# Kernel optimization log

Measured on AMD Instinct MI355X. Metric: run time of the kernel, lower is better.

The kernel has to match this reference:

```python
import jax, jax.numpy as jnp
import numpy as np

B, N = 64, 512
D_ENT, H = 2000, 768
LN_EPS = 1e-12


def setup_inputs() -> dict:
    key = jax.random.key(0)
    ks = jax.random.split(key, 16)
    s = 1.0 / np.sqrt(D_ENT)
    sh = 1.0 / np.sqrt(H)
    return {
        "node_embeddings": jax.random.normal(ks[0], (B, N, D_ENT), jnp.float32),
        "node_types": jax.random.randint(ks[1], (B, N), 0, 2),
        "layers": jax.random.randint(ks[2], (B, N), 0, 8),
        "operators": jax.random.randint(ks[3], (B, N), 0, 2),
        "in_degs": jax.random.randint(ks[4], (B, N), 0, 8),
        "out_degs": jax.random.randint(ks[5], (B, N), 0, 8),
        "negs": jax.random.randint(ks[6], (B, N), 0, 2),
        "type_emb": jax.random.normal(ks[7], (2, H), jnp.float32),
        "layer_emb": jax.random.normal(ks[8], (8, H), jnp.float32),
        "op_emb": jax.random.normal(ks[9], (2, H), jnp.float32),
        "in_emb": jax.random.normal(ks[10], (8, H), jnp.float32),
        "out_emb": jax.random.normal(ks[11], (8, H), jnp.float32),
        "proj_w": jax.random.uniform(ks[12], (H, D_ENT), jnp.float32, -s, s),
        "proj_b": jnp.zeros((H,), jnp.float32),
        "neg_w": jax.random.uniform(ks[13], (H, H), jnp.float32, -sh, sh),
        "neg_b": jnp.zeros((H,), jnp.float32),
        "ln_g": jnp.ones((H,), jnp.float32),
        "ln_b": jnp.zeros((H,), jnp.float32),
    }


def reference(node_embeddings, node_types, layers, operators, in_degs, out_degs, negs,
              type_emb, layer_emb, op_emb, in_emb, out_emb,
              proj_w, proj_b, neg_w, neg_b, ln_g, ln_b):
    # linear projection: [B,N,D_ENT] @ [D_ENT,H]
    x = jnp.einsum("bnd,hd->bnh", node_embeddings, proj_w) + proj_b
    # summed small-table lookups
    x = x + type_emb[node_types] + layer_emb[layers] + op_emb[operators] \
        + in_emb[in_degs] + out_emb[out_degs]
    # rows with negs==1 go through MLP (single Linear h->h); masked select/scatter
    y = jnp.einsum("bnh,gh->bng", x, neg_w) + neg_b
    x = jnp.where((negs == 1)[..., None], y, x)
    # LayerNorm
    mu = jnp.mean(x, axis=-1, keepdims=True)
    var = jnp.mean(jnp.square(x - mu), axis=-1, keepdims=True)
    x = (x - mu) * jax.lax.rsqrt(var + LN_EPS) * ln_g + ln_b
    # dropout is identity in eval mode
    return x
```

## Files before the change

kernel.cpp:

```cpp
#include <hip/hip_runtime.h>
#include <stdint.h>

typedef unsigned short u16;
typedef short v8s __attribute__((ext_vector_type(8)));
typedef float v4f __attribute__((ext_vector_type(4)));

typedef __attribute__((address_space(1))) uint32_t g_u32;
typedef __attribute__((address_space(3))) uint32_t l_u32;

__device__ __forceinline__ void glds16(const void* g, void* l) {
    __builtin_amdgcn_global_load_lds((const g_u32*)g, (l_u32*)l, 16, 0, 0);
}

__device__ __forceinline__ u16 f2b(float f) {
    uint32_t u = __builtin_bit_cast(uint32_t, f);
    u += 0x7FFFu + ((u >> 16) & 1u);
    return (u16)(u >> 16);
}

__device__ __forceinline__ uint32_t pk2(float a, float b) {
    uint32_t ua = __builtin_bit_cast(uint32_t, a) + 0x8000u;
    uint32_t ub = __builtin_bit_cast(uint32_t, b) + 0x8000u;
    return __builtin_amdgcn_perm(ub, ua, 0x07060302u);
}

#define MTOT  32768
#define HDIM  768
#define KDIM  2000
#define KPAD  2016

__global__ __launch_bounds__(256) void cvt_weights(
    const float* __restrict__ pw, const float* __restrict__ nw,
    u16* __restrict__ Wb, u16* __restrict__ NWb)
{
    const int h = blockIdx.x;
    const float* src = pw + (size_t)h * KDIM;
    u16* dst = Wb + (size_t)h * KPAD;
    for (int k = threadIdx.x; k < KPAD; k += 256)
        dst[k] = (k < KDIM) ? f2b(src[k]) : (u16)0;
    const float* s2 = nw + (size_t)h * HDIM;
    u16* d2 = NWb + (size_t)h * HDIM;
    for (int k = threadIdx.x; k < HDIM; k += 256)
        d2[k] = f2b(s2[k]);
}

__global__ __launch_bounds__(256, 3) void gemm1(
    const float* __restrict__ A, const u16* __restrict__ Wb,
    const float* __restrict__ pb,
    const int* __restrict__ i_ty, const int* __restrict__ i_la,
    const int* __restrict__ i_op, const int* __restrict__ i_in, const int* __restrict__ i_ou,
    const float* __restrict__ te, const float* __restrict__ le, const float* __restrict__ oe,
    const float* __restrict__ ie, const float* __restrict__ ooe,
    u16* __restrict__ Xb)
{
    __shared__ __align__(16) float Asf[128 * 32];
    __shared__ __align__(16) u16  Bs[128 * 32];

    const int bid = blockIdx.x;
    const int slot = bid >> 3;
    const int mt = (bid & 7) * 32 + slot / 6;
    const int nt = slot % 6;
    const int m_base = mt * 128, n_base = nt * 128;

    const int tid = threadIdx.x;
    const int w = tid >> 6, lane = tid & 63;
    const int lm = lane & 15, quad = lane >> 4;
    const int wm = (w >> 1) * 64, wn = (w & 1) * 64;

    const float* aRowBase[4];
    int aChunkOff[4];
    float* aDst[4];
#pragma unroll
    for (int t = 0; t < 4; t++) {
        const int rl = w * 32 + t * 8 + (lane >> 3);
        const int c16 = (lane & 7) ^ (rl & 7);
        aRowBase[t] = A + (size_t)(m_base + rl) * KDIM;
        aChunkOff[t] = c16 * 4;
        aDst[t] = &Asf[(w * 32 + t * 8) * 32];
    }
    const u16* bSrc[2];
    u16* bDst[2];
#pragma unroll
    for (int t = 0; t < 2; t++) {
        const int rl = w * 32 + t * 16 + (lane >> 2);
        const int c = (lane & 3) ^ ((rl >> 1) & 3);
        bSrc[t] = Wb + (size_t)(n_base + rl) * KPAD + c * 8;
        bDst[t] = &Bs[(w * 32 + t * 16) * 32];
    }

    v4f acc[4][4];
#pragma unroll
    for (int i = 0; i < 4; i++)
#pragma unroll
        for (int j = 0; j < 4; j++) acc[i][j] = (v4f){0.f, 0.f, 0.f, 0.f};

    for (int kb = 0; kb < KPAD / 32; ++kb) {
        __syncthreads();
#pragma unroll
        for (int t = 0; t < 4; t++) {
            int k = kb * 32 + aChunkOff[t];
            k = (k > 1996) ? 1996 : k;
            glds16(aRowBase[t] + k, aDst[t]);
        }
#pragma unroll
        for (int t = 0; t < 2; t++)
            glds16(bSrc[t] + kb * 32, bDst[t]);
        __syncthreads();

        v8s af[4], bf[4];
#pragma unroll
        for (int i = 0; i < 4; i++) {
            const int r = wm + i * 16 + lm;
            const int sw = r & 7;
            const float4 lo = *(const float4*)&Asf[r * 32 + (((2 * quad)     ^ sw) << 2)];
            const float4 hi = *(const float4*)&Asf[r * 32 + (((2 * quad + 1) ^ sw) << 2)];
            int4 p;
            p.x = (int)pk2(lo.x, lo.y); p.y = (int)pk2(lo.z, lo.w);
            p.z = (int)pk2(hi.x, hi.y); p.w = (int)pk2(hi.z, hi.w);
            af[i] = __builtin_bit_cast(v8s, p);
        }
#pragma unroll
        for (int j = 0; j < 4; j++) {
            const int r = wn + j * 16 + lm;
            bf[j] = *(const v8s*)&Bs[r * 32 + (quad ^ ((r >> 1) & 3)) * 8];
        }
#pragma unroll
        for (int i = 0; i < 4; i++)
#pragma unroll
            for (int j = 0; j < 4; j++)
                acc[i][j] = __builtin_amdgcn_mfma_f32_16x16x32_bf16(af[i], bf[j], acc[i][j], 0, 0, 0);
    }

#pragma unroll
    for (int i = 0; i < 4; i++) {
#pragma unroll
        for (int r = 0; r < 4; r++) {
            const int row = m_base + wm + i * 16 + quad * 4 + r;
            const int ty = i_ty[row], la = i_la[row], op = i_op[row];
            const int di = i_in[row], doo = i_ou[row];
            const float* pte = te + (size_t)ty * HDIM;
            const float* ple = le + (size_t)la * HDIM;
            const float* poe = oe + (size_t)op * HDIM;
            const float* pie = ie + (size_t)di * HDIM;
            const float* pou = ooe + (size_t)doo * HDIM;
            u16* orow = Xb + (size_t)row * HDIM;
#pragma unroll
            for (int j = 0; j < 4; j++) {
                const int col = n_base + wn + j * 16 + lm;
                float v = acc[i][j][r] + pb[col] + pte[col] + ple[col] + poe[col] + pie[col] + pou[col];
                orow[col] = f2b(v);
            }
        }
    }
}

__global__ __launch_bounds__(256, 3) void gemm2(
    const u16* __restrict__ Xb, const u16* __restrict__ NWb,
    const float* __restrict__ nb, u16* __restrict__ Yb)
{
    __shared__ __align__(16) u16 As[128 * 32];
    __shared__ __align__(16) u16 Bs[128 * 32];

    const int bid = blockIdx.x;
    const int slot = bid >> 3;
    const int mt = (bid & 7) * 32 + slot / 6;
    const int nt = slot % 6;
    const int m_base = mt * 128, n_base = nt * 128;

    const int tid = threadIdx.x;
    const int w = tid >> 6, lane = tid & 63;
    const int lm = lane & 15, quad = lane >> 4;
    const int wm = (w >> 1) * 64, wn = (w & 1) * 64;

    const u16* aSrc[2]; u16* aDst[2];
    const u16* bSrc[2]; u16* bDst[2];
#pragma unroll
    for (int t = 0; t < 2; t++) {
        const int rl = w * 32 + t * 16 + (lane >> 2);
        const int c = (lane & 3) ^ ((rl >> 1) & 3);
        aSrc[t] = Xb  + (size_t)(m_base + rl) * HDIM + c * 8;
        aDst[t] = &As[(w * 32 + t * 16) * 32];
        bSrc[t] = NWb + (size_t)(n_base + rl) * HDIM + c * 8;
        bDst[t] = &Bs[(w * 32 + t * 16) * 32];
    }

    v4f acc[4][4];
#pragma unroll
    for (int i = 0; i < 4; i++)
#pragma unroll
        for (int j = 0; j < 4; j++) acc[i][j] = (v4f){0.f, 0.f, 0.f, 0.f};

    for (int kb = 0; kb < HDIM / 32; ++kb) {
        __syncthreads();
#pragma unroll
        for (int t = 0; t < 2; t++) {
            glds16(aSrc[t] + kb * 32, aDst[t]);
            glds16(bSrc[t] + kb * 32, bDst[t]);
        }
        __syncthreads();

        v8s af[4], bf[4];
#pragma unroll
        for (int i = 0; i < 4; i++) {
            const int r = wm + i * 16 + lm;
            af[i] = *(const v8s*)&As[r * 32 + (quad ^ ((r >> 1) & 3)) * 8];
        }
#pragma unroll
        for (int j = 0; j < 4; j++) {
            const int r = wn + j * 16 + lm;
            bf[j] = *(const v8s*)&Bs[r * 32 + (quad ^ ((r >> 1) & 3)) * 8];
        }
#pragma unroll
        for (int i = 0; i < 4; i++)
#pragma unroll
            for (int j = 0; j < 4; j++)
                acc[i][j] = __builtin_amdgcn_mfma_f32_16x16x32_bf16(af[i], bf[j], acc[i][j], 0, 0, 0);
    }

#pragma unroll
    for (int i = 0; i < 4; i++) {
#pragma unroll
        for (int r = 0; r < 4; r++) {
            const int row = m_base + wm + i * 16 + quad * 4 + r;
            u16* orow = Yb + (size_t)row * HDIM;
#pragma unroll
            for (int j = 0; j < 4; j++) {
                const int col = n_base + wn + j * 16 + lm;
                orow[col] = f2b(acc[i][j][r] + nb[col]);
            }
        }
    }
}

__global__ __launch_bounds__(256) void ln_k(
    const u16* __restrict__ Xb, const u16* __restrict__ Yb,
    const int* __restrict__ negs,
    const float* __restrict__ g, const float* __restrict__ b,
    float* __restrict__ out)
{
    const int w = threadIdx.x >> 6, lane = threadIdx.x & 63;
    const int row = blockIdx.x * 4 + w;
    const u16* src = ((negs[row] == 1) ? Yb : Xb) + (size_t)row * HDIM;

    float v[12];
    float s = 0.f, ss = 0.f;
#pragma unroll
    for (int p = 0; p < 3; p++) {
        uint2 u = *(const uint2*)(src + (p * 64 + lane) * 4);
        float f0 = __builtin_bit_cast(float, u.x << 16);
        float f1 = __builtin_bit_cast(float, u.x & 0xFFFF0000u);
        float f2 = __builtin_bit_cast(float, u.y << 16);
        float f3 = __builtin_bit_cast(float, u.y & 0xFFFF0000u);
        v[p * 4 + 0] = f0; v[p * 4 + 1] = f1; v[p * 4 + 2] = f2; v[p * 4 + 3] = f3;
        s += f0 + f1 + f2 + f3;
        ss += f0 * f0 + f1 * f1 + f2 * f2 + f3 * f3;
    }
#pragma unroll
    for (int off = 1; off < 64; off <<= 1) {
        s += __shfl_xor(s, off);
        ss += __shfl_xor(ss, off);
    }
    const float mean = s * (1.f / (float)HDIM);
    const float var = ss * (1.f / (float)HDIM) - mean * mean;
    const float rs = rsqrtf(var + 1e-12f);

    float* orow = out + (size_t)row * HDIM;
#pragma unroll
    for (int p = 0; p < 3; p++) {
        const int c0 = (p * 64 + lane) * 4;
        float4 gg = *(const float4*)(g + c0);
        float4 bb = *(const float4*)(b + c0);
        float4 o;
        o.x = (v[p * 4 + 0] - mean) * rs * gg.x + bb.x;
        o.y = (v[p * 4 + 1] - mean) * rs * gg.y + bb.y;
        o.z = (v[p * 4 + 2] - mean) * rs * gg.z + bb.z;
        o.w = (v[p * 4 + 3] - mean) * rs * gg.w + bb.w;
        *(float4*)(orow + c0) = o;
    }
}

extern "C" void kernel_launch(void* const* d_in, const int* in_sizes, int n_in,
                              void* d_out, int out_size, void* d_ws, size_t ws_size,
                              hipStream_t stream) {
    (void)in_sizes; (void)n_in; (void)out_size; (void)ws_size;
    const float* A   = (const float*)d_in[0];
    const int* i_ty  = (const int*)d_in[1];
    const int* i_la  = (const int*)d_in[2];
    const int* i_op  = (const int*)d_in[3];
    const int* i_in  = (const int*)d_in[4];
    const int* i_ou  = (const int*)d_in[5];
    const int* negs  = (const int*)d_in[6];
    const float* te  = (const float*)d_in[7];
    const float* le  = (const float*)d_in[8];
    const float* oe  = (const float*)d_in[9];
    const float* ie  = (const float*)d_in[10];
    const float* ooe = (const float*)d_in[11];
    const float* pw  = (const float*)d_in[12];
    const float* pb  = (const float*)d_in[13];
    const float* nw  = (const float*)d_in[14];
    const float* nb  = (const float*)d_in[15];
    const float* lng = (const float*)d_in[16];
    const float* lnb = (const float*)d_in[17];
    float* out = (float*)d_out;

    char* ws = (char*)d_ws;
    u16* Wb  = (u16*)ws;
    u16* NWb = (u16*)(ws + 3096576);
    u16* Xb  = (u16*)(ws + 3096576 + 1179648);
    u16* Yb  = (u16*)(ws + 3096576 + 1179648 + 50331648);

    cvt_weights<<<768, 256, 0, stream>>>(pw, nw, Wb, NWb);
    gemm1<<<1536, 256, 0, stream>>>(A, Wb, pb, i_ty, i_la, i_op, i_in, i_ou,
                                    te, le, oe, ie, ooe, Xb);
    gemm2<<<1536, 256, 0, stream>>>(Xb, NWb, nb, Yb);
    ln_k<<<8192, 256, 0, stream>>>(Xb, Yb, negs, lng, lnb, out);
}
```

Baseline: 676.8 us.

## Pre-convert activations to bf16 in a separate pass before the projection GEMM

Adds a kernel that converts the fp32 node embeddings to bf16 in workspace. The projection GEMM then streams bf16 tiles straight into LDS and drops the per-iteration fp32-to-bf16 packing, halving both the A-tile LDS footprint and the global read volume across the N-tiles. The change also raises the occupancy hint from 3 to 4 for both GEMMs. The cost is an extra full read and write pass over the large input. The old fused path stays as a fallback when the workspace is too small.

```diff
diff --git a/kernel.cpp b/kernel.cpp
--- a/kernel.cpp
+++ b/kernel.cpp
@@ -28,6 +28,24 @@
 #define HDIM  768
 #define KDIM  2000
 #define KPAD  2016
+
+__global__ __launch_bounds__(256) void cvt_a(
+    const float* __restrict__ A, u16* __restrict__ Ab)
+{
+    const int t = threadIdx.x;
+    if (t >= 250) return;
+#pragma unroll
+    for (int r = 0; r < 8; r++) {
+        const int row = blockIdx.x * 8 + r;
+        const float* src = A + (size_t)row * KDIM + t * 8;
+        const float4 a = ((const float4*)src)[0];
+        const float4 b = ((const float4*)src)[1];
+        int4 p;
+        p.x = (int)pk2(a.x, a.y); p.y = (int)pk2(a.z, a.w);
+        p.z = (int)pk2(b.x, b.y); p.w = (int)pk2(b.z, b.w);
+        *(int4*)(Ab + (size_t)row * KDIM + t * 8) = p;
+    }
+}
 
 __global__ __launch_bounds__(256) void cvt_weights(
     const float* __restrict__ pw, const float* __restrict__ nw,
@@ -44,8 +62,8 @@
         d2[k] = f2b(s2[k]);
 }
 
-__global__ __launch_bounds__(256, 3) void gemm1(
-    const float* __restrict__ A, const u16* __restrict__ Wb,
+__global__ __launch_bounds__(256, 4) void gemm1(
+    const u16* __restrict__ Ab, const u16* __restrict__ Wb,
     const float* __restrict__ pb,
     const int* __restrict__ i_ty, const int* __restrict__ i_la,
     const int* __restrict__ i_op, const int* __restrict__ i_in, const int* __restrict__ i_ou,
@@ -53,8 +71,8 @@
     const float* __restrict__ ie, const float* __restrict__ ooe,
     u16* __restrict__ Xb)
 {
-    __shared__ __align__(16) float Asf[128 * 32];
-    __shared__ __align__(16) u16  Bs[128 * 32];
+    __shared__ __align__(16) u16 As[128 * 32];
+    __shared__ __align__(16) u16 Bs[128 * 32];
 
     const int bid = blockIdx.x;
     const int slot = bid >> 3;
@@ -67,25 +85,17 @@
     const int lm = lane & 15, quad = lane >> 4;
     const int wm = (w >> 1) * 64, wn = (w & 1) * 64;
 
-    const float* aRowBase[4];
-    int aChunkOff[4];
-    float* aDst[4];
-#pragma unroll
-    for (int t = 0; t < 4; t++) {
-        const int rl = w * 32 + t * 8 + (lane >> 3);
-        const int c16 = (lane & 7) ^ (rl & 7);
-        aRowBase[t] = A + (size_t)(m_base + rl) * KDIM;
-        aChunkOff[t] = c16 * 4;
-        aDst[t] = &Asf[(w * 32 + t * 8) * 32];
-    }
-    const u16* bSrc[2];
-    u16* bDst[2];
+    const u16* aRow[2]; int aOff[2]; u16* aDst[2];
+    const u16* bSrc[2]; u16* bDst[2];
 #pragma unroll
     for (int t = 0; t < 2; t++) {
         const int rl = w * 32 + t * 16 + (lane >> 2);
         const int c = (lane & 3) ^ ((rl >> 1) & 3);
+        aRow[t] = Ab + (size_t)(m_base + rl) * KDIM;
+        aOff[t] = c * 8;
+        aDst[t] = (u16*)&As[(w * 32 + t * 16) * 32];
         bSrc[t] = Wb + (size_t)(n_base + rl) * KPAD + c * 8;
-        bDst[t] = &Bs[(w * 32 + t * 16) * 32];
+        bDst[t] = (u16*)&Bs[(w * 32 + t * 16) * 32];
     }
 
     v4f acc[4][4];
@@ -97,27 +107,19 @@
     for (int kb = 0; kb < KPAD / 32; ++kb) {
         __syncthreads();
 #pragma unroll
-        for (int t = 0; t < 4; t++) {
-            int k = kb * 32 + aChunkOff[t];
-            k = (k > 1996) ? 1996 : k;
-            glds16(aRowBase[t] + k, aDst[t]);
-        }
-#pragma unroll
-        for (int t = 0; t < 2; t++)
+        for (int t = 0; t < 2; t++) {
+            int k = kb * 32 + aOff[t];
+            k = (k > 1992) ? 1992 : k;
+            glds16(aRow[t] + k, aDst[t]);
             glds16(bSrc[t] + kb * 32, bDst[t]);
+        }
         __syncthreads();
 
         v8s af[4], bf[4];
 #pragma unroll
         for (int i = 0; i < 4; i++) {
             const int r = wm + i * 16 + lm;
-            const int sw = r & 7;
-            const float4 lo = *(const float4*)&Asf[r * 32 + (((2 * quad)     ^ sw) << 2)];
-            const float4 hi = *(const float4*)&Asf[r * 32 + (((2 * quad + 1) ^ sw) << 2)];
-            int4 p;
-            p.x = (int)pk2(lo.x, lo.y); p.y = (int)pk2(lo.z, lo.w);
-            p.z = (int)pk2(hi.x, hi.y); p.w = (int)pk2(hi.z, hi.w);
-            af[i] = __builtin_bit_cast(v8s, p);
+            af[i] = *(const v8s*)&As[r * 32 + (quad ^ ((r >> 1) & 3)) * 8];
         }
 #pragma unroll
         for (int j = 0; j < 4; j++) {
@@ -154,7 +156,114 @@
     }
 }
 
-__global__ __launch_bounds__(256, 3) void gemm2(
+__global__ __launch_bounds__(256, 3) void gemm1_fused(
+    const float* __restrict__ A, const u16* __restrict__ Wb,
+    const float* __restrict__ pb,
+    const int* __restrict__ i_ty, const int* __restrict__ i_la,
+    const int* __restrict__ i_op, const int* __restrict__ i_in, const int* __restrict__ i_ou,
+    const float* __restrict__ te, const float* __restrict__ le, const float* __restrict__ oe,
+    const float* __restrict__ ie, const float* __restrict__ ooe,
+    u16* __restrict__ Xb)
+{
+    __shared__ __align__(16) float Asf[128 * 32];
+    __shared__ __align__(16) u16  Bs[128 * 32];
+
+    const int bid = blockIdx.x;
+    const int slot = bid >> 3;
+    const int mt = (bid & 7) * 32 + slot / 6;
+    const int nt = slot % 6;
+    const int m_base = mt * 128, n_base = nt * 128;
+
+    const int tid = threadIdx.x;
+    const int w = tid >> 6, lane = tid & 63;
+    const int lm = lane & 15, quad = lane >> 4;
+    const int wm = (w >> 1) * 64, wn = (w & 1) * 64;
+
+    const float* aRowBase[4]; int aChunkOff[4]; float* aDst[4];
+#pragma unroll
+    for (int t = 0; t < 4; t++) {
+        const int rl = w * 32 + t * 8 + (lane >> 3);
+        const int c16 = (lane & 7) ^ (rl & 7);
+        aRowBase[t] = A + (size_t)(m_base + rl) * KDIM;
+        aChunkOff[t] = c16 * 4;
+        aDst[t] = &Asf[(w * 32 + t * 8) * 32];
+    }
+    const u16* bSrc[2]; u16* bDst[2];
+#pragma unroll
+    for (int t = 0; t < 2; t++) {
+        const int rl = w * 32 + t * 16 + (lane >> 2);
+        const int c = (lane & 3) ^ ((rl >> 1) & 3);
+        bSrc[t] = Wb + (size_t)(n_base + rl) * KPAD + c * 8;
+        bDst[t] = &Bs[(w * 32 + t * 16) * 32];
+    }
+
+    v4f acc[4][4];
+#pragma unroll
+    for (int i = 0; i < 4; i++)
+#pragma unroll
+        for (int j = 0; j < 4; j++) acc[i][j] = (v4f){0.f, 0.f, 0.f, 0.f};
+
+    for (int kb = 0; kb < KPAD / 32; ++kb) {
+        __syncthreads();
+#pragma unroll
+        for (int t = 0; t < 4; t++) {
+            int k = kb * 32 + aChunkOff[t];
+            k = (k > 1996) ? 1996 : k;
+            glds16(aRowBase[t] + k, aDst[t]);
+        }
+#pragma unroll
+        for (int t = 0; t < 2; t++)
+            glds16(bSrc[t] + kb * 32, bDst[t]);
+        __syncthreads();
+
+        v8s af[4], bf[4];
+#pragma unroll
+        for (int i = 0; i < 4; i++) {
+            const int r = wm + i * 16 + lm;
+            const int sw = r & 7;
+            const float4 lo = *(const float4*)&Asf[r * 32 + (((2 * quad)     ^ sw) << 2)];
+            const float4 hi = *(const float4*)&Asf[r * 32 + (((2 * quad + 1) ^ sw) << 2)];
+            int4 p;
+            p.x = (int)pk2(lo.x, lo.y); p.y = (int)pk2(lo.z, lo.w);
+            p.z = (int)pk2(hi.x, hi.y); p.w = (int)pk2(hi.z, hi.w);
+            af[i] = __builtin_bit_cast(v8s, p);
+        }
+#pragma unroll
+        for (int j = 0; j < 4; j++) {
+            const int r = wn + j * 16 + lm;
+            bf[j] = *(const v8s*)&Bs[r * 32 + (quad ^ ((r >> 1) & 3)) * 8];
+        }
+#pragma unroll
+        for (int i = 0; i < 4; i++)
+#pragma unroll
+            for (int j = 0; j < 4; j++)
+                acc[i][j] = __builtin_amdgcn_mfma_f32_16x16x32_bf16(af[i], bf[j], acc[i][j], 0, 0, 0);
+    }
+
+#pragma unroll
+    for (int i = 0; i < 4; i++) {
+#pragma unroll
+        for (int r = 0; r < 4; r++) {
+            const int row = m_base + wm + i * 16 + quad * 4 + r;
+            const int ty = i_ty[row], la = i_la[row], op = i_op[row];
+            const int di = i_in[row], doo = i_ou[row];
+            const float* pte = te + (size_t)ty * HDIM;
+            const float* ple = le + (size_t)la * HDIM;
+            const float* poe = oe + (size_t)op * HDIM;
+            const float* pie = ie + (size_t)di * HDIM;
+            const float* pou = ooe + (size_t)doo * HDIM;
+            u16* orow = Xb + (size_t)row * HDIM;
+#pragma unroll
+            for (int j = 0; j < 4; j++) {
+                const int col = n_base + wn + j * 16 + lm;
+                float v = acc[i][j][r] + pb[col] + pte[col] + ple[col] + poe[col] + pie[col] + pou[col];
+                orow[col] = f2b(v);
+            }
+        }
+    }
+}
+
+__global__ __launch_bounds__(256, 4) void gemm2(
     const u16* __restrict__ Xb, const u16* __restrict__ NWb,
     const float* __restrict__ nb, u16* __restrict__ Yb)
 {
@@ -282,7 +391,7 @@
 extern "C" void kernel_launch(void* const* d_in, const int* in_sizes, int n_in,
                               void* d_out, int out_size, void* d_ws, size_t ws_size,
                               hipStream_t stream) {
-    (void)in_sizes; (void)n_in; (void)out_size; (void)ws_size;
+    (void)in_sizes; (void)n_in; (void)out_size;
     const float* A   = (const float*)d_in[0];
     const int* i_ty  = (const int*)d_in[1];
     const int* i_la  = (const int*)d_in[2];
@@ -304,14 +413,27 @@
     float* out = (float*)d_out;
 
     char* ws = (char*)d_ws;
-    u16* Wb  = (u16*)ws;
-    u16* NWb = (u16*)(ws + 3096576);
-    u16* Xb  = (u16*)(ws + 3096576 + 1179648);
-    u16* Yb  = (u16*)(ws + 3096576 + 1179648 + 50331648);
+    const size_t oWb  = 0;
+    const size_t oNWb = oWb  + (size_t)768 * KPAD * 2;
+    const size_t oXb  = oNWb + (size_t)768 * HDIM * 2;
+    const size_t oYb  = oXb  + (size_t)MTOT * HDIM * 2;
+    const size_t oAb  = oYb  + (size_t)MTOT * HDIM * 2;
+    const size_t need = oAb  + (size_t)MTOT * KDIM * 2;
+    u16* Wb  = (u16*)(ws + oWb);
+    u16* NWb = (u16*)(ws + oNWb);
+    u16* Xb  = (u16*)(ws + oXb);
+    u16* Yb  = (u16*)(ws + oYb);
+    u16* Ab  = (u16*)(ws + oAb);
 
     cvt_weights<<<768, 256, 0, stream>>>(pw, nw, Wb, NWb);
-    gemm1<<<1536, 256, 0, stream>>>(A, Wb, pb, i_ty, i_la, i_op, i_in, i_ou,
-                                    te, le, oe, ie, ooe, Xb);
+    if (ws_size >= need) {
+        cvt_a<<<4096, 256, 0, stream>>>(A, Ab);
+        gemm1<<<1536, 256, 0, stream>>>(Ab, Wb, pb, i_ty, i_la, i_op, i_in, i_ou,
+                                        te, le, oe, ie, ooe, Xb);
+    } else {
+        gemm1_fused<<<1536, 256, 0, stream>>>(A, Wb, pb, i_ty, i_la, i_op, i_in, i_ou,
+                                              te, le, oe, ie, ooe, Xb);
+    }
     gemm2<<<1536, 256, 0, stream>>>(Xb, NWb, nb, Yb);
     ln_k<<<8192, 256, 0, stream>>>(Xb, Yb, negs, lng, lnb, out);
 }
```

New measurement: 702.9 us. +3.9%, slower.
